# Kernel tuning notes

Hardware: AMD Instinct MI355X
Metric: run time of the kernel (lower is better)

## Reference

```python
import jax, jax.numpy as jnp
import numpy as np

B, N, D = 2, 8192, 128
TEMP_MIN = 1e-4


def setup_inputs() -> dict:
    key = jax.random.key(0)
    k0, k1 = jax.random.split(key)
    feats0 = jax.random.normal(k0, (B, N, D), dtype=jnp.float32)
    feats1 = jax.random.normal(k1, (B, N, D), dtype=jnp.float32)
    temp = jnp.ones((), dtype=jnp.float32)  # nn.Parameter(temp_init=1.0)
    return {"feats0": feats0, "feats1": feats1, "temp": temp}


def reference(feats0, feats1, temp):
    x2 = jnp.sum(feats0 * feats0, axis=-1, keepdims=True)            # [B, N0, 1]
    y2 = jnp.sum(feats1 * feats1, axis=-1, keepdims=True)            # [B, N1, 1]
    dists = x2 - 2.0 * jnp.einsum('bnd,bmd->bnm', feats0, feats1)
    dists = dists + jnp.swapaxes(y2, -2, -1)                          # [B, N0, N1]

    t = jnp.maximum(temp * temp, TEMP_MIN)                            # get_temp()
    probs = jax.nn.softmax(-dists / t, axis=-1)                       # [B, N0, N1]

    idx = jnp.argmax(probs, axis=-1)                                  # [B, N0]
    asgn = jax.nn.one_hot(idx, probs.shape[-1], dtype=probs.dtype)    # hard one-hot
    # straight-through: value = one-hot, gradient = softmax gradient
    asgn_diff = asgn - jax.lax.stop_gradient(probs) + probs
    return asgn_diff, idx
```

## Files before the change

kernel.cpp:

```cpp
#include <hip/hip_runtime.h>
#include <hip/hip_fp16.h>
#include <cstdint>
#include <cstddef>

#define NPTS 8192
#define DDIM 128
#define BATCH 2
#define NROWS (BATCH * NPTS)
#define EPSGAP 1.0f
#define NCOLT 64
#define WCAP 512

typedef __attribute__((ext_vector_type(8))) _Float16 half8v;
typedef __attribute__((ext_vector_type(4))) float f32x4;

typedef __attribute__((address_space(3))) unsigned int as3_uint;
typedef const __attribute__((address_space(1))) unsigned int as1_uint;

__global__ void split_kernel(const float* __restrict__ f0, const float* __restrict__ f1,
                             unsigned short* __restrict__ Aext, unsigned short* __restrict__ Bext,
                             float* __restrict__ y2, unsigned int* __restrict__ flagCount) {
    if (blockIdx.x == 0 && threadIdx.x == 0) *flagCount = 0u;
    const unsigned half = gridDim.x >> 1;
    const bool isB = blockIdx.x >= half;
    const float* src = isB ? f1 : f0;
    unsigned short* dst = isB ? Bext : Aext;
    size_t t = (size_t)(blockIdx.x - (isB ? half : 0)) * 256 + threadIdx.x;
    size_t row = t >> 5;
    int kc = (int)(t & 31) * 4;
    float4 v = reinterpret_cast<const float4*>(src)[t];
    ushort4 h;
    h.x = __half_as_ushort(__float2half(v.x));
    h.y = __half_as_ushort(__float2half(v.y));
    h.z = __half_as_ushort(__float2half(v.z));
    h.w = __half_as_ushort(__float2half(v.w));
    *reinterpret_cast<ushort4*>(&dst[row * 128 + kc]) = h;

    if (isB) {
        float s = fmaf(v.x, v.x, fmaf(v.y, v.y, fmaf(v.z, v.z, v.w * v.w)));
#pragma unroll
        for (int off = 16; off >= 1; off >>= 1) s += __shfl_xor(s, off);
        if ((t & 31) == 0) y2[row] = s;
    }
}

__global__ __launch_bounds__(256) void gemm_mfma(
    const unsigned short* __restrict__ Aext,
    const unsigned short* __restrict__ Bext,
    const float* __restrict__ y2g,
    float* __restrict__ pv1, float* __restrict__ pv2, unsigned int* __restrict__ pidx,
    float* __restrict__ outZero)
{
    __shared__ __align__(16) short As[128 * 64];
    __shared__ __align__(16) short Bs[128 * 64];
    __shared__ float rv1[2][128];
    __shared__ float rv2[2][128];
    __shared__ unsigned int ri[2][128];

    const unsigned flat = blockIdx.x;
    const unsigned wg   = (flat & 7u) * 1024u + (flat >> 3);
    const int bm  = wg & 63;
    const int bnc = (int)((wg >> 6) & 63);
    const int b   = (int)(wg >> 12);

    const int tid  = threadIdx.x;
    const int lane = tid & 63;
    const int wid  = tid >> 6;
    const int wr   = wid >> 1, wc = wid & 1;
    const int l15  = lane & 15, l4 = lane >> 4;
    const int row0 = bm * 128, col0 = bnc * 128;

    const unsigned short* Abase = Aext + ((size_t)b * NPTS + row0) * 128;
    const unsigned short* Bbase = Bext + ((size_t)b * NPTS + col0) * 128;

    f32x4 acc[4][4];
#pragma unroll
    for (int i = 0; i < 4; ++i)
#pragma unroll
        for (int j = 0; j < 4; ++j) acc[i][j] = (f32x4)0.0f;

#pragma unroll
    for (int kk = 0; kk < 2; ++kk) {
        __syncthreads();
        {
            const int ko = kk * 64;
#pragma unroll
            for (int it = 0; it < 4; ++it) {
                int flat2 = it * 256 + tid;
                int r = flat2 >> 3, kc = flat2 & 7;
                int kcs = kc ^ (r & 7);
                const unsigned short* ga = Abase + (size_t)r * 128 + ko + kcs * 8;
                const unsigned short* gb = Bbase + (size_t)r * 128 + ko + kcs * 8;
                __builtin_amdgcn_global_load_lds((as1_uint*)ga, (as3_uint*)&As[flat2 * 8], 16, 0, 0);
                __builtin_amdgcn_global_load_lds((as1_uint*)gb, (as3_uint*)&Bs[flat2 * 8], 16, 0, 0);
            }
        }
        __syncthreads();
#pragma unroll
        for (int ks = 0; ks < 2; ++ks) {
            half8v a[4], bf[4];
#pragma unroll
            for (int i = 0; i < 4; ++i) {
                int ra = wr * 64 + i * 16 + l15;
                int ch = ks * 4 + l4;
                a[i] = *reinterpret_cast<const half8v*>(&As[ra * 64 + ((ch ^ (ra & 7)) << 3)]);
            }
#pragma unroll
            for (int j = 0; j < 4; ++j) {
                int rb = wc * 64 + j * 16 + l15;
                int ch = ks * 4 + l4;
                bf[j] = *reinterpret_cast<const half8v*>(&Bs[rb * 64 + ((ch ^ (rb & 7)) << 3)]);
            }
#pragma unroll
            for (int i = 0; i < 4; ++i)
#pragma unroll
                for (int j = 0; j < 4; ++j)
                    acc[i][j] = __builtin_amdgcn_mfma_f32_16x16x32_f16(a[i], bf[j], acc[i][j], 0, 0, 0);
        }
    }

    const float* y2b = y2g + b * NPTS;
    float yv[4];
#pragma unroll
    for (int j = 0; j < 4; ++j) yv[j] = y2b[col0 + wc * 64 + j * 16 + l15];

    {
        f32x4* o4 = reinterpret_cast<f32x4*>(outZero) + (size_t)wg * 4096;
        const f32x4 z = (f32x4)0.0f;
#pragma unroll
        for (int it = 0; it < 16; ++it)
            __builtin_nontemporal_store(z, &o4[it * 256 + tid]);
    }

#pragma unroll
    for (int i = 0; i < 4; ++i) {
#pragma unroll
        for (int q = 0; q < 4; ++q) {
            float v1 = INFINITY, v2 = INFINITY;
            unsigned int mi = 0u;
#pragma unroll
            for (int j = 0; j < 4; ++j) {
                const float v = fmaf(-2.0f, acc[i][j][q], yv[j]);
                const unsigned int m = (unsigned)(col0 + wc * 64 + j * 16 + l15);
                if (v < v1) { v2 = v1; v1 = v; mi = m; }
                else        { v2 = fminf(v2, v); }
            }
#pragma unroll
            for (int off = 1; off < 16; off <<= 1) {
                float o1 = __shfl_xor(v1, off);
                float o2 = __shfl_xor(v2, off);
                unsigned int oi = __shfl_xor(mi, off);
                if (o1 < v1 || (o1 == v1 && oi < mi)) { v2 = fminf(v1, o2); v1 = o1; mi = oi; }
                else                                  { v2 = fminf(v2, fminf(o1, o2)); }
            }
            if (l15 == 0) {
                const int rl = wr * 64 + i * 16 + l4 * 4 + q;
                rv1[wc][rl] = v1; rv2[wc][rl] = v2; ri[wc][rl] = mi;
            }
        }
    }
    __syncthreads();
    if (tid < 128) {
        float a1 = rv1[0][tid], a2 = rv2[0][tid];
        unsigned int ai = ri[0][tid];
        const float o1 = rv1[1][tid], o2 = rv2[1][tid];
        const unsigned int oi = ri[1][tid];
        if (o1 < a1 || (o1 == a1 && oi < ai)) { a2 = fminf(a1, o2); a1 = o1; ai = oi; }
        else                                  { a2 = fminf(a2, fminf(o1, o2)); }
        const size_t gr = (size_t)b * NPTS + row0 + tid;
        pv1[(size_t)bnc * NROWS + gr] = a1;
        pv2[(size_t)bnc * NROWS + gr] = a2;
        pidx[(size_t)bnc * NROWS + gr] = ai;
    }
}

__global__ void resolve_kernel(const float* __restrict__ pv1, const float* __restrict__ pv2,
                               const unsigned int* __restrict__ pidx,
                               float* __restrict__ bestval, float* __restrict__ out,
                               unsigned int* __restrict__ flagList, unsigned int* __restrict__ flagCount)
{
    const int gr = blockIdx.x * 256 + threadIdx.x;
    float a1 = INFINITY, a2 = INFINITY;
    unsigned int ai = 0u;
    for (int cs = 0; cs < NCOLT; ++cs) {
        const float o1 = pv1[(size_t)cs * NROWS + gr];
        const float o2 = pv2[(size_t)cs * NROWS + gr];
        const unsigned int oi = pidx[(size_t)cs * NROWS + gr];
        if (o1 < a1 || (o1 == a1 && oi < ai)) { a2 = fminf(a1, o2); a1 = o1; ai = oi; }
        else                                  { a2 = fminf(a2, fminf(o1, o2)); }
    }
    bestval[gr] = a1;
    if (a2 - a1 < EPSGAP) {
        unsigned int pos = atomicAdd(flagCount, 1u);
        flagList[pos] = (unsigned int)gr;
    } else {
        out[(size_t)gr * NPTS + ai] = 1.0f;
        out[(size_t)BATCH * NPTS * NPTS + gr] = (float)ai;
    }
}

__global__ __launch_bounds__(256) void recheck_kernel(
    const float* __restrict__ f0, const float* __restrict__ f1,
    const float* __restrict__ pv1, const float* __restrict__ pv2,
    const unsigned int* __restrict__ pidx, const float* __restrict__ bestval,
    const unsigned int* __restrict__ flagList, const unsigned int* __restrict__ flagCount,
    float* __restrict__ out)
{
    __shared__ float xrow[4][DDIM];
    __shared__ unsigned int cand[4][WCAP];
    __shared__ int ncand[4];

    const int tid  = threadIdx.x;
    const int w    = tid >> 6;
    const int lane = tid & 63;
    const unsigned int nflag = *flagCount;
    const unsigned int slot0 = blockIdx.x * 4 + w;
    const unsigned int nslots = gridDim.x * 4;

    for (unsigned int li = slot0; li < nflag; li += nslots) {
        const int gr = (int)flagList[li];
        const int b = gr >> 13, n = gr & (NPTS - 1);
        const float W = bestval[gr] + EPSGAP;

        if (lane == 0) ncand[w] = 0;
        const float* xp = f0 + ((size_t)b * NPTS + n) * DDIM;
        xrow[w][lane]      = xp[lane];
        xrow[w][lane + 64] = xp[lane + 64];

        {
            const size_t base = (size_t)lane * NROWS + gr;
            const float t1 = pv1[base];
            if (t1 <= W) {
                if (pv2[base] <= W) {
                    int p = atomicAdd(&ncand[w], 128);
                    if (p + 128 <= WCAP)
                        for (int c = 0; c < 128; ++c) cand[w][p + c] = (unsigned)(lane * 128 + c);
                } else {
                    int p = atomicAdd(&ncand[w], 1);
                    if (p < WCAP) cand[w][p] = pidx[base];
                }
            }
        }
        asm volatile("s_waitcnt lgkmcnt(0)" ::: "memory");

        const int nc = ncand[w];
        double bv = 1e300;
        unsigned int bi = 0xFFFFFFFFu;
        const float4* xpv = reinterpret_cast<const float4*>(xrow[w]);
        if (nc <= WCAP) {
            for (int c = lane; c < nc; c += 64) {
                const unsigned int m = cand[w][c];
                const float4* ypv = reinterpret_cast<const float4*>(f1 + ((size_t)b * NPTS + m) * DDIM);
                double s0 = 0.0, s1 = 0.0, s2 = 0.0, s3 = 0.0;
#pragma unroll 8
                for (int k4 = 0; k4 < DDIM / 4; ++k4) {
                    const float4 y = ypv[k4];
                    const float4 x = xpv[k4];
                    s0 = fma((double)y.x, (double)y.x - 2.0 * (double)x.x, s0);
                    s1 = fma((double)y.y, (double)y.y - 2.0 * (double)x.y, s1);
                    s2 = fma((double)y.z, (double)y.z - 2.0 * (double)x.z, s2);
                    s3 = fma((double)y.w, (double)y.w - 2.0 * (double)x.w, s3);
                }
                const double v = (s0 + s1) + (s2 + s3);
                if (v < bv || (v == bv && m < bi)) { bv = v; bi = m; }
            }
        } else {
            for (int m = lane; m < NPTS; m += 64) {
                const float4* ypv = reinterpret_cast<const float4*>(f1 + ((size_t)b * NPTS + m) * DDIM);
                double s0 = 0.0, s1 = 0.0, s2 = 0.0, s3 = 0.0;
#pragma unroll 4
                for (int k4 = 0; k4 < DDIM / 4; ++k4) {
                    const float4 y = ypv[k4];
                    const float4 x = xpv[k4];
                    s0 = fma((double)y.x, (double)y.x - 2.0 * (double)x.x, s0);
                    s1 = fma((double)y.y, (double)y.y - 2.0 * (double)x.y, s1);
                    s2 = fma((double)y.z, (double)y.z - 2.0 * (double)x.z, s2);
                    s3 = fma((double)y.w, (double)y.w - 2.0 * (double)x.w, s3);
                }
                const double v = (s0 + s1) + (s2 + s3);
                if (v < bv || (v == bv && (unsigned)m < bi)) { bv = v; bi = (unsigned)m; }
            }
        }
#pragma unroll
        for (int off = 1; off < 64; off <<= 1) {
            const double ov = __shfl_xor(bv, off);
            const unsigned int oi = __shfl_xor(bi, off);
            if (ov < bv || (ov == bv && oi < bi)) { bv = ov; bi = oi; }
        }
        if (lane == 0) {
            out[(size_t)gr * NPTS + bi] = 1.0f;
            out[(size_t)BATCH * NPTS * NPTS + gr] = (float)bi;
        }
        asm volatile("s_waitcnt lgkmcnt(0)" ::: "memory");
    }
}

extern "C" void kernel_launch(void* const* d_in, const int* in_sizes, int n_in,
                              void* d_out, int out_size, void* d_ws, size_t ws_size,
                              hipStream_t stream)
{
    const float* f0 = (const float*)d_in[0];
    const float* f1 = (const float*)d_in[1];
    float* out = (float*)d_out;

    char* wsb = (char*)d_ws;
    unsigned short* Aext = (unsigned short*)wsb;                  wsb += (size_t)BATCH * NPTS * 128 * 2;
    unsigned short* Bext = (unsigned short*)wsb;                  wsb += (size_t)BATCH * NPTS * 128 * 2;
    float* y2            = (float*)wsb;                           wsb += (size_t)NROWS * 4;
    float* pv1           = (float*)wsb;                           wsb += (size_t)NCOLT * NROWS * 4;
    float* pv2           = (float*)wsb;                           wsb += (size_t)NCOLT * NROWS * 4;
    unsigned int* pidx   = (unsigned int*)wsb;                    wsb += (size_t)NCOLT * NROWS * 4;
    float* bestval       = (float*)wsb;                           wsb += (size_t)NROWS * 4;
    unsigned int* flagList = (unsigned int*)wsb;                  wsb += (size_t)NROWS * 4;
    unsigned int* flagCount = (unsigned int*)wsb;

    split_kernel<<<2 * (BATCH * NPTS * 32) / 256, 256, 0, stream>>>(f0, f1, Aext, Bext, y2, flagCount);
    gemm_mfma<<<NPTS / 128 * NPTS / 128 * BATCH, 256, 0, stream>>>(Aext, Bext, y2, pv1, pv2, pidx, out);
    resolve_kernel<<<NROWS / 256, 256, 0, stream>>>(pv1, pv2, pidx, bestval, out, flagList, flagCount);
    recheck_kernel<<<512, 256, 0, stream>>>(f0, f1, pv1, pv2, pidx, bestval, flagList, flagCount, out);
}
```

Measured before the change: 207.5 us.

## Fuse fp32-to-fp16 conversion and row norms into the MFMA GEMM kernel

Removes the separate split kernel and instead has each GEMM workgroup load fp32 features directly, convert them to fp16 in registers, and write them into swizzled LDS. The squared norms of the feats1 rows are accumulated during the load and reduced through shuffles into shared memory, and the GEMM kernel now resets the flag counter. This saves one kernel launch and the fp16 workspace round trip. In exchange, each tile reads twice as many bytes from global memory, every tile redoes the conversion, and the async global-to-LDS loads become synchronous register staging. The recheck kernel grid is also doubled.

Result: slower. 316.2 us (+52.3%).

```diff
diff --git a/kernel.cpp b/kernel.cpp
--- a/kernel.cpp
+++ b/kernel.cpp
@@ -14,48 +14,17 @@
 typedef __attribute__((ext_vector_type(8))) _Float16 half8v;
 typedef __attribute__((ext_vector_type(4))) float f32x4;
 
-typedef __attribute__((address_space(3))) unsigned int as3_uint;
-typedef const __attribute__((address_space(1))) unsigned int as1_uint;
-
-__global__ void split_kernel(const float* __restrict__ f0, const float* __restrict__ f1,
-                             unsigned short* __restrict__ Aext, unsigned short* __restrict__ Bext,
-                             float* __restrict__ y2, unsigned int* __restrict__ flagCount) {
-    if (blockIdx.x == 0 && threadIdx.x == 0) *flagCount = 0u;
-    const unsigned half = gridDim.x >> 1;
-    const bool isB = blockIdx.x >= half;
-    const float* src = isB ? f1 : f0;
-    unsigned short* dst = isB ? Bext : Aext;
-    size_t t = (size_t)(blockIdx.x - (isB ? half : 0)) * 256 + threadIdx.x;
-    size_t row = t >> 5;
-    int kc = (int)(t & 31) * 4;
-    float4 v = reinterpret_cast<const float4*>(src)[t];
-    ushort4 h;
-    h.x = __half_as_ushort(__float2half(v.x));
-    h.y = __half_as_ushort(__float2half(v.y));
-    h.z = __half_as_ushort(__float2half(v.z));
-    h.w = __half_as_ushort(__float2half(v.w));
-    *reinterpret_cast<ushort4*>(&dst[row * 128 + kc]) = h;
-
-    if (isB) {
-        float s = fmaf(v.x, v.x, fmaf(v.y, v.y, fmaf(v.z, v.z, v.w * v.w)));
-#pragma unroll
-        for (int off = 16; off >= 1; off >>= 1) s += __shfl_xor(s, off);
-        if ((t & 31) == 0) y2[row] = s;
-    }
-}
-
 __global__ __launch_bounds__(256) void gemm_mfma(
-    const unsigned short* __restrict__ Aext,
-    const unsigned short* __restrict__ Bext,
-    const float* __restrict__ y2g,
+    const float* __restrict__ f0, const float* __restrict__ f1,
     float* __restrict__ pv1, float* __restrict__ pv2, unsigned int* __restrict__ pidx,
-    float* __restrict__ outZero)
+    float* __restrict__ outZero, unsigned int* __restrict__ flagCount)
 {
     __shared__ __align__(16) short As[128 * 64];
     __shared__ __align__(16) short Bs[128 * 64];
     __shared__ float rv1[2][128];
     __shared__ float rv2[2][128];
     __shared__ unsigned int ri[2][128];
+    __shared__ float y2s[128];
 
     const unsigned flat = blockIdx.x;
     const unsigned wg   = (flat & 7u) * 1024u + (flat >> 3);
@@ -70,14 +39,20 @@
     const int l15  = lane & 15, l4 = lane >> 4;
     const int row0 = bm * 128, col0 = bnc * 128;
 
-    const unsigned short* Abase = Aext + ((size_t)b * NPTS + row0) * 128;
-    const unsigned short* Bbase = Bext + ((size_t)b * NPTS + col0) * 128;
+    if (flat == 0 && tid == 0) *flagCount = 0u;
+
+    const float* f0b = f0 + ((size_t)b * NPTS + row0) * DDIM;
+    const float* f1b = f1 + ((size_t)b * NPTS + col0) * DDIM;
 
     f32x4 acc[4][4];
 #pragma unroll
     for (int i = 0; i < 4; ++i)
 #pragma unroll
         for (int j = 0; j < 4; ++j) acc[i][j] = (f32x4)0.0f;
+
+    float y2acc[8];
+#pragma unroll
+    for (int it = 0; it < 8; ++it) y2acc[it] = 0.0f;
 
 #pragma unroll
     for (int kk = 0; kk < 2; ++kk) {
@@ -85,14 +60,25 @@
         {
             const int ko = kk * 64;
 #pragma unroll
-            for (int it = 0; it < 4; ++it) {
-                int flat2 = it * 256 + tid;
-                int r = flat2 >> 3, kc = flat2 & 7;
-                int kcs = kc ^ (r & 7);
-                const unsigned short* ga = Abase + (size_t)r * 128 + ko + kcs * 8;
-                const unsigned short* gb = Bbase + (size_t)r * 128 + ko + kcs * 8;
-                __builtin_amdgcn_global_load_lds((as1_uint*)ga, (as3_uint*)&As[flat2 * 8], 16, 0, 0);
-                __builtin_amdgcn_global_load_lds((as1_uint*)gb, (as3_uint*)&Bs[flat2 * 8], 16, 0, 0);
+            for (int it = 0; it < 8; ++it) {
+                const int flat2 = it * 256 + tid;
+                const int r  = flat2 >> 4;
+                const int c4 = flat2 & 15;
+                const float4 va = *reinterpret_cast<const float4*>(&f0b[(size_t)r * DDIM + ko + c4 * 4]);
+                const float4 vb = *reinterpret_cast<const float4*>(&f1b[(size_t)r * DDIM + ko + c4 * 4]);
+                ushort4 ha, hb;
+                ha.x = __half_as_ushort(__float2half(va.x));
+                ha.y = __half_as_ushort(__float2half(va.y));
+                ha.z = __half_as_ushort(__float2half(va.z));
+                ha.w = __half_as_ushort(__float2half(va.w));
+                hb.x = __half_as_ushort(__float2half(vb.x));
+                hb.y = __half_as_ushort(__float2half(vb.y));
+                hb.z = __half_as_ushort(__float2half(vb.z));
+                hb.w = __half_as_ushort(__float2half(vb.w));
+                const int su = ((((c4 >> 1) ^ (r & 7)) << 1) | (c4 & 1));
+                *reinterpret_cast<ushort4*>(&As[r * 64 + su * 4]) = ha;
+                *reinterpret_cast<ushort4*>(&Bs[r * 64 + su * 4]) = hb;
+                y2acc[it] = fmaf(vb.x, vb.x, fmaf(vb.y, vb.y, fmaf(vb.z, vb.z, fmaf(vb.w, vb.w, y2acc[it]))));
             }
         }
         __syncthreads();
@@ -119,10 +105,14 @@
         }
     }
 
-    const float* y2b = y2g + b * NPTS;
-    float yv[4];
-#pragma unroll
-    for (int j = 0; j < 4; ++j) yv[j] = y2b[col0 + wc * 64 + j * 16 + l15];
+#pragma unroll
+    for (int it = 0; it < 8; ++it) {
+        float s = y2acc[it];
+        s += __shfl_xor(s, 1); s += __shfl_xor(s, 2);
+        s += __shfl_xor(s, 4); s += __shfl_xor(s, 8);
+        const int flat2 = it * 256 + tid;
+        if ((flat2 & 15) == 0) y2s[flat2 >> 4] = s;
+    }
 
     {
         f32x4* o4 = reinterpret_cast<f32x4*>(outZero) + (size_t)wg * 4096;
@@ -131,6 +121,11 @@
         for (int it = 0; it < 16; ++it)
             __builtin_nontemporal_store(z, &o4[it * 256 + tid]);
     }
+
+    __syncthreads();
+    float yv[4];
+#pragma unroll
+    for (int j = 0; j < 4; ++j) yv[j] = y2s[wc * 64 + j * 16 + l15];
 
 #pragma unroll
     for (int i = 0; i < 4; ++i) {
@@ -304,9 +299,6 @@
     float* out = (float*)d_out;
 
     char* wsb = (char*)d_ws;
-    unsigned short* Aext = (unsigned short*)wsb;                  wsb += (size_t)BATCH * NPTS * 128 * 2;
-    unsigned short* Bext = (unsigned short*)wsb;                  wsb += (size_t)BATCH * NPTS * 128 * 2;
-    float* y2            = (float*)wsb;                           wsb += (size_t)NROWS * 4;
     float* pv1           = (float*)wsb;                           wsb += (size_t)NCOLT * NROWS * 4;
     float* pv2           = (float*)wsb;                           wsb += (size_t)NCOLT * NROWS * 4;
     unsigned int* pidx   = (unsigned int*)wsb;                    wsb += (size_t)NCOLT * NROWS * 4;
@@ -314,8 +306,7 @@
     unsigned int* flagList = (unsigned int*)wsb;                  wsb += (size_t)NROWS * 4;
     unsigned int* flagCount = (unsigned int*)wsb;
 
-    split_kernel<<<2 * (BATCH * NPTS * 32) / 256, 256, 0, stream>>>(f0, f1, Aext, Bext, y2, flagCount);
-    gemm_mfma<<<NPTS / 128 * NPTS / 128 * BATCH, 256, 0, stream>>>(Aext, Bext, y2, pv1, pv2, pidx, out);
+    gemm_mfma<<<NPTS / 128 * NPTS / 128 * BATCH, 256, 0, stream>>>(f0, f1, pv1, pv2, pidx, out, flagCount);
     resolve_kernel<<<NROWS / 256, 256, 0, stream>>>(pv1, pv2, pidx, bestval, out, flagList, flagCount);
-    recheck_kernel<<<512, 256, 0, stream>>>(f0, f1, pv1, pv2, pidx, bestval, flagList, flagCount, out);
+    recheck_kernel<<<1024, 256, 0, stream>>>(f0, f1, pv1, pv2, pidx, bestval, flagList, flagCount, out);
 }
```

## Fuse resolve and recheck into one kernel; move part of zero-fill into split

Applied to the files above, without the earlier changes.

Merges the resolve and recheck kernels into one finalize kernel. Each block reduces 64 rows using 4 threads per row with shuffle merges, and rechecks its ambiguous rows locally through shared memory. This removes the global flag list, the global atomic counter and one kernel launch. It also moves the zero-fill of part of the output from the GEMM blocks with wg >= ZSPLIT into the A-half blocks of the split kernel, to balance store traffic. The risk is load imbalance, since blocks that hit many ambiguous rows recheck them serially with only 4 waves.

Result: slower. 228.7 us (+10.2%).

```diff
diff --git a/kernel.cpp b/kernel.cpp
--- a/kernel.cpp
+++ b/kernel.cpp
@@ -10,6 +10,7 @@
 #define EPSGAP 1.0f
 #define NCOLT 64
 #define WCAP 512
+#define ZSPLIT 6144
 
 typedef __attribute__((ext_vector_type(8))) _Float16 half8v;
 typedef __attribute__((ext_vector_type(4))) float f32x4;
@@ -19,8 +20,7 @@
 
 __global__ void split_kernel(const float* __restrict__ f0, const float* __restrict__ f1,
                              unsigned short* __restrict__ Aext, unsigned short* __restrict__ Bext,
-                             float* __restrict__ y2, unsigned int* __restrict__ flagCount) {
-    if (blockIdx.x == 0 && threadIdx.x == 0) *flagCount = 0u;
+                             float* __restrict__ y2, float* __restrict__ outZero) {
     const unsigned half = gridDim.x >> 1;
     const bool isB = blockIdx.x >= half;
     const float* src = isB ? f1 : f0;
@@ -41,6 +41,12 @@
 #pragma unroll
         for (int off = 16; off >= 1; off >>= 1) s += __shfl_xor(s, off);
         if ((t & 31) == 0) y2[row] = s;
+    } else {
+        f32x4* o4 = reinterpret_cast<f32x4*>(outZero) + ((size_t)ZSPLIT + blockIdx.x) * 4096;
+        const f32x4 z = (f32x4)0.0f;
+#pragma unroll
+        for (int it = 0; it < 16; ++it)
+            __builtin_nontemporal_store(z, &o4[it * 256 + threadIdx.x]);
     }
 }
 
@@ -124,7 +130,7 @@
 #pragma unroll
     for (int j = 0; j < 4; ++j) yv[j] = y2b[col0 + wc * 64 + j * 16 + l15];
 
-    {
+    if (wg < ZSPLIT) {
         f32x4* o4 = reinterpret_cast<f32x4*>(outZero) + (size_t)wg * 4096;
         const f32x4 z = (f32x4)0.0f;
 #pragma unroll
@@ -174,53 +180,71 @@
     }
 }
 
-__global__ void resolve_kernel(const float* __restrict__ pv1, const float* __restrict__ pv2,
-                               const unsigned int* __restrict__ pidx,
-                               float* __restrict__ bestval, float* __restrict__ out,
-                               unsigned int* __restrict__ flagList, unsigned int* __restrict__ flagCount)
-{
-    const int gr = blockIdx.x * 256 + threadIdx.x;
-    float a1 = INFINITY, a2 = INFINITY;
-    unsigned int ai = 0u;
-    for (int cs = 0; cs < NCOLT; ++cs) {
-        const float o1 = pv1[(size_t)cs * NROWS + gr];
-        const float o2 = pv2[(size_t)cs * NROWS + gr];
-        const unsigned int oi = pidx[(size_t)cs * NROWS + gr];
-        if (o1 < a1 || (o1 == a1 && oi < ai)) { a2 = fminf(a1, o2); a1 = o1; ai = oi; }
-        else                                  { a2 = fminf(a2, fminf(o1, o2)); }
-    }
-    bestval[gr] = a1;
-    if (a2 - a1 < EPSGAP) {
-        unsigned int pos = atomicAdd(flagCount, 1u);
-        flagList[pos] = (unsigned int)gr;
-    } else {
-        out[(size_t)gr * NPTS + ai] = 1.0f;
-        out[(size_t)BATCH * NPTS * NPTS + gr] = (float)ai;
-    }
-}
-
-__global__ __launch_bounds__(256) void recheck_kernel(
+__global__ __launch_bounds__(256) void finalize_kernel(
     const float* __restrict__ f0, const float* __restrict__ f1,
     const float* __restrict__ pv1, const float* __restrict__ pv2,
-    const unsigned int* __restrict__ pidx, const float* __restrict__ bestval,
-    const unsigned int* __restrict__ flagList, const unsigned int* __restrict__ flagCount,
+    const unsigned int* __restrict__ pidx,
     float* __restrict__ out)
 {
     __shared__ float xrow[4][DDIM];
     __shared__ unsigned int cand[4][WCAP];
     __shared__ int ncand[4];
-
-    const int tid  = threadIdx.x;
+    __shared__ float s_best[64];
+    __shared__ unsigned char s_flag[64];
+    __shared__ int s_nflag;
+
+    const int tid = threadIdx.x;
+    const int gr0 = blockIdx.x * 64;
+
+    if (tid == 0) s_nflag = 0;
+    __syncthreads();
+
+    {
+        const int r  = tid >> 2;
+        const int q  = tid & 3;
+        const int gr = gr0 + r;
+        float a1 = INFINITY, a2 = INFINITY;
+        unsigned int ai = 0u;
+#pragma unroll 4
+        for (int c = 0; c < 16; ++c) {
+            const int cs = q * 16 + c;
+            const size_t base = (size_t)cs * NROWS + gr;
+            const float o1 = pv1[base];
+            const float o2 = pv2[base];
+            const unsigned int oi = pidx[base];
+            if (o1 < a1 || (o1 == a1 && oi < ai)) { a2 = fminf(a1, o2); a1 = o1; ai = oi; }
+            else                                  { a2 = fminf(a2, fminf(o1, o2)); }
+        }
+#pragma unroll
+        for (int off = 1; off < 4; off <<= 1) {
+            const float o1 = __shfl_xor(a1, off);
+            const float o2 = __shfl_xor(a2, off);
+            const unsigned int oi = __shfl_xor(ai, off);
+            if (o1 < a1 || (o1 == a1 && oi < ai)) { a2 = fminf(a1, o2); a1 = o1; ai = oi; }
+            else                                  { a2 = fminf(a2, fminf(o1, o2)); }
+        }
+        if (q == 0) {
+            if (a2 - a1 < EPSGAP) {
+                const int p = atomicAdd(&s_nflag, 1);
+                s_flag[p] = (unsigned char)r;
+                s_best[r] = a1;
+            } else {
+                out[(size_t)gr * NPTS + ai] = 1.0f;
+                out[(size_t)BATCH * NPTS * NPTS + gr] = (float)ai;
+            }
+        }
+    }
+    __syncthreads();
+
+    const int nf   = s_nflag;
     const int w    = tid >> 6;
     const int lane = tid & 63;
-    const unsigned int nflag = *flagCount;
-    const unsigned int slot0 = blockIdx.x * 4 + w;
-    const unsigned int nslots = gridDim.x * 4;
-
-    for (unsigned int li = slot0; li < nflag; li += nslots) {
-        const int gr = (int)flagList[li];
+
+    for (int li = w; li < nf; li += 4) {
+        const int rr = (int)s_flag[li];
+        const int gr = gr0 + rr;
         const int b = gr >> 13, n = gr & (NPTS - 1);
-        const float W = bestval[gr] + EPSGAP;
+        const float W = s_best[rr] + EPSGAP;
 
         if (lane == 0) ncand[w] = 0;
         const float* xp = f0 + ((size_t)b * NPTS + n) * DDIM;
@@ -309,13 +333,9 @@
     float* y2            = (float*)wsb;                           wsb += (size_t)NROWS * 4;
     float* pv1           = (float*)wsb;                           wsb += (size_t)NCOLT * NROWS * 4;
     float* pv2           = (float*)wsb;                           wsb += (size_t)NCOLT * NROWS * 4;
-    unsigned int* pidx   = (unsigned int*)wsb;                    wsb += (size_t)NCOLT * NROWS * 4;
-    float* bestval       = (float*)wsb;                           wsb += (size_t)NROWS * 4;
-    unsigned int* flagList = (unsigned int*)wsb;                  wsb += (size_t)NROWS * 4;
-    unsigned int* flagCount = (unsigned int*)wsb;
-
-    split_kernel<<<2 * (BATCH * NPTS * 32) / 256, 256, 0, stream>>>(f0, f1, Aext, Bext, y2, flagCount);
+    unsigned int* pidx   = (unsigned int*)wsb;
+
+    split_kernel<<<2 * (BATCH * NPTS * 32) / 256, 256, 0, stream>>>(f0, f1, Aext, Bext, y2, out);
     gemm_mfma<<<NPTS / 128 * NPTS / 128 * BATCH, 256, 0, stream>>>(Aext, Bext, y2, pv1, pv2, pidx, out);
-    resolve_kernel<<<NROWS / 256, 256, 0, stream>>>(pv1, pv2, pidx, bestval, out, flagList, flagCount);
-    recheck_kernel<<<512, 256, 0, stream>>>(f0, f1, pv1, pv2, pidx, bestval, flagList, flagCount, out);
+    finalize_kernel<<<NROWS / 64, 256, 0, stream>>>(f0, f1, pv1, pv2, pidx, out);
 }
```
